# Performance work log

Measured on AMD Instinct MI355X. Metric: run time of the kernel, lower is better.

The kernel has to match this reference:

```python
import jax, jax.numpy as jnp
import numpy as np

B, N, D = 8, 2048, 256
C = 8192  # codebook_size
H = 1     # num_codebooks


def setup_inputs() -> dict:
    key = jax.random.key(0)
    k1, k2 = jax.random.split(key)
    x = jax.random.normal(k1, (B, N, D), dtype=jnp.float32)
    # kaiming_uniform_ on [H, C, D]: bound = sqrt(6 / fan_in), fan_in = C*D for a 3D tensor
    bound = float(np.sqrt(6.0 / (C * D)))
    embed = jax.random.uniform(k2, (H, C, D), dtype=jnp.float32, minval=-bound, maxval=bound)
    return {"x": x, "embed": embed}


def reference(x, embed):
    # x: [B, N, D]; module adds a codebook dim since ndim < 4, flattens to [H, B*N, D]
    flat = x.reshape(1, -1, x.shape[-1]).astype(jnp.float32)  # [H, M, D], M = B*N
    # squared euclidean distance (argmin identical to argmin of cdist p=2)
    x2 = jnp.sum(flat * flat, axis=-1, keepdims=True)              # [H, M, 1]
    e2 = jnp.sum(embed * embed, axis=-1)[:, None, :]               # [H, 1, C]
    xe = jnp.einsum('hmd,hcd->hmc', flat, embed)                   # [H, M, C]
    d2 = x2 - 2.0 * xe + e2                                        # [H, M, C]
    # sample_codebook_temp == 0 -> pure argmax of -dist == argmin of dist
    ind = jnp.argmin(d2, axis=-1)                                  # [H, M]
    quantize = jnp.take(embed[0], ind[0], axis=0).reshape(x.shape) # [B, N, D]
    embed_ind = ind.reshape(x.shape[:-1])                          # [B, N]
    return quantize, embed_ind
```

## Files before the change

### kernel.cpp

```cpp
#include <hip/hip_runtime.h>
#include <hip/hip_bf16.h>

#define M_TOT 16384
#define D_DIM 256
#define C_TOT 8192
#define NCH 4
#define CCH (C_TOT / NCH)
#define QOFF (M_TOT * D_DIM)
#define NPART 8

typedef _Float16 f16;
typedef __attribute__((ext_vector_type(8))) _Float16 f16x8;
typedef __attribute__((ext_vector_type(4))) float f32x4;

#define WS_X2 0
#define WS_E2 (M_TOT)
#define WS_BV (M_TOT + C_TOT)
#define WS_BI (WS_BV + NPART * M_TOT)
#define WS_SPL (WS_BI + NPART * M_TOT)
#define XH_OFF ((size_t)0)
#define XL_OFF ((size_t)M_TOT * D_DIM)
#define EH_OFF ((size_t)2 * M_TOT * D_DIM)
#define EL_OFF ((size_t)2 * M_TOT * D_DIM + (size_t)C_TOT * D_DIM)
#define SPL_HALFS ((size_t)2 * M_TOT * D_DIM + (size_t)2 * C_TOT * D_DIM)
#define WS_NEED ((size_t)WS_SPL * 4 + SPL_HALFS * 2)

__device__ __forceinline__ void gll16(const void* g, void* l) {
    __builtin_amdgcn_global_load_lds((const __attribute__((address_space(1))) void*)g,
                                     (__attribute__((address_space(3))) void*)l, 16, 0, 0);
}

__global__ void split_kernel(const float* __restrict__ x, const float* __restrict__ e,
                             f16* __restrict__ sp, float* __restrict__ x2, float* __restrict__ e2)
{
    int row  = blockIdx.x * 4 + (threadIdx.x >> 6);
    int lane = threadIdx.x & 63;
    bool isx = row < M_TOT;
    int r = isx ? row : row - M_TOT;
    const float* src = (isx ? x : e) + (size_t)r * D_DIM;
    float4 v = *(const float4*)(src + lane * 4);
    float s = v.x * v.x + v.y * v.y + v.z * v.z + v.w * v.w;
    #pragma unroll
    for (int off = 32; off >= 1; off >>= 1) s += __shfl_xor(s, off, 64);
    float sc = isx ? 256.0f : 16384.0f;
    float a[4] = {v.x * sc, v.y * sc, v.z * sc, v.w * sc};
    union { f16 h[4]; ushort4 u; } hh, ll;
    #pragma unroll
    for (int i = 0; i < 4; ++i) {
        f16 h = (f16)a[i];
        hh.h[i] = h;
        ll.h[i] = (f16)(a[i] - (float)h);
    }
    size_t base = (size_t)r * D_DIM + lane * 4;
    f16* ph = sp + (isx ? XH_OFF : EH_OFF) + base;
    f16* pl = sp + (isx ? XL_OFF : EL_OFF) + base;
    *(ushort4*)ph = hh.u;
    *(ushort4*)pl = ll.u;
    if (lane == 0) { if (isx) x2[r] = s; else e2[r] = s; }
}

__global__ __launch_bounds__(512, 2) void mdist_kernel(
    const f16* __restrict__ sp, const float* __restrict__ x2, const float* __restrict__ e2,
    float* __restrict__ bestv, int* __restrict__ besti)
{
    __shared__ __align__(16) f16 lds[65536];

    const int t  = threadIdx.x;
    const int l  = t & 63;
    const int wv = t >> 6;
    const int wr = wv >> 1, wc = wv & 1;
    const int mt = (int)blockIdx.x >> 2;
    const int ch = (int)blockIdx.x & 3;
    const int m0 = mt * 256, c0 = ch * CCH;

    const int q  = l >> 4;
    const int fr = l & 15;

    const int wvh = wv >> 2, rb = wv & 3;
    const f16* gxh = sp + XH_OFF + (size_t)(m0 + rb * 64 + l) * D_DIM;
    const f16* gxl = sp + XL_OFF + (size_t)(m0 + rb * 64 + l) * D_DIM;
    const f16* geh = sp + EH_OFF + (size_t)(c0 + rb * 64 + l) * D_DIM;
    const f16* gel = sp + EL_OFF + (size_t)(c0 + rb * 64 + l) * D_DIM;
    char* lbase = (char*)&lds[0] + rb * 1024 + l * 16;

#define KB(it) ((2 * (it) + wvh) & 3)
    auto STAGE = [&](int buf, int ktv, int ctv) {
        const size_t ko = (size_t)ktv * 32;
        const size_t co = (size_t)ctv * 256 * D_DIM + ko;
        char* lb = lbase + buf * 65536;
        gll16(gxh + ko + KB(0) * 8, lb + 0 * 16384 + KB(0) * 4096);
        gll16(gxh + ko + KB(1) * 8, lb + 0 * 16384 + KB(1) * 4096);
        gll16(gxl + ko + KB(2) * 8, lb + 1 * 16384 + KB(2) * 4096);
        gll16(gxl + ko + KB(3) * 8, lb + 1 * 16384 + KB(3) * 4096);
        gll16(geh + co + KB(4) * 8, lb + 2 * 16384 + KB(4) * 4096);
        gll16(geh + co + KB(5) * 8, lb + 2 * 16384 + KB(5) * 4096);
        gll16(gel + co + KB(6) * 8, lb + 3 * 16384 + KB(6) * 4096);
        gll16(gel + co + KB(7) * 8, lb + 3 * 16384 + KB(7) * 4096);
    };

    float bst[16]; int bix[16];
    #pragma unroll
    for (int i = 0; i < 16; ++i) { bst[i] = 3.4e38f; bix[i] = 0; }

    STAGE(0, 0, 0);

    for (int ct = 0; ct < 8; ++ct) {
        const int cb = c0 + ct * 256;
        f32x4 acc[4][8];
        #pragma unroll
        for (int m = 0; m < 4; ++m)
            #pragma unroll
            for (int n = 0; n < 8; ++n)
                #pragma unroll
                for (int k = 0; k < 4; ++k) acc[m][n][k] = 0.f;

        #pragma unroll 1
        for (int kt = 0; kt < 8; ++kt) {
            const int cur = kt & 1;
            asm volatile("s_waitcnt vmcnt(0)" ::: "memory");
            __syncthreads();
            __builtin_amdgcn_sched_barrier(0);

            if (kt < 7)       STAGE(cur ^ 1, kt + 1, ct);
            else if (ct < 7)  STAGE(cur ^ 1, 0, ct + 1);

            const f16* L = &lds[0] + cur * 32768;

            f16x8 ah[4], al[4];
            #pragma unroll
            for (int m = 0; m < 4; ++m) {
                int aoff = (q * 256 + wr * 64 + m * 16 + fr) * 8;
                ah[m] = *(const f16x8*)(L + aoff);
                al[m] = *(const f16x8*)(L + 8192 + aoff);
            }
            #pragma unroll
            for (int n = 0; n < 8; ++n) {
                int boff = (q * 256 + wc * 128 + n * 16 + fr) * 8;
                f16x8 bhn = *(const f16x8*)(L + 16384 + boff);
                f16x8 bln = *(const f16x8*)(L + 24576 + boff);
                __builtin_amdgcn_s_setprio(1);
                #pragma unroll
                for (int m = 0; m < 4; ++m)
                    acc[m][n] = __builtin_amdgcn_mfma_f32_16x16x32_f16(ah[m], bhn, acc[m][n], 0, 0, 0);
                #pragma unroll
                for (int m = 0; m < 4; ++m)
                    acc[m][n] = __builtin_amdgcn_mfma_f32_16x16x32_f16(ah[m], bln, acc[m][n], 0, 0, 0);
                #pragma unroll
                for (int m = 0; m < 4; ++m)
                    acc[m][n] = __builtin_amdgcn_mfma_f32_16x16x32_f16(al[m], bhn, acc[m][n], 0, 0, 0);
                __builtin_amdgcn_s_setprio(0);
            }
        }

        float e2v[8];
        #pragma unroll
        for (int n = 0; n < 8; ++n) e2v[n] = e2[cb + wc * 128 + n * 16 + fr];
        #pragma unroll
        for (int m = 0; m < 4; ++m) {
            f32x4 x2v = *(const f32x4*)(x2 + m0 + wr * 64 + m * 16 + q * 4);
            #pragma unroll
            for (int j = 0; j < 4; ++j) {
                const int bi = m * 4 + j;
                #pragma unroll
                for (int n = 0; n < 8; ++n) {
                    float d = fmaf(acc[m][n][j], -0x1p-21f, x2v[j]) + e2v[n];
                    int c = cb + wc * 128 + n * 16 + fr;
                    if (d < bst[bi]) { bst[bi] = d; bix[bi] = c; }
                }
            }
        }
    }

    #pragma unroll
    for (int i = 0; i < 16; ++i) {
        float v = bst[i]; int idx = bix[i];
        #pragma unroll
        for (int off = 8; off >= 1; off >>= 1) {
            float ov = __shfl_xor(v, off, 64);
            int   oi = __shfl_xor(idx, off, 64);
            if (ov < v || (ov == v && oi < idx)) { v = ov; idx = oi; }
        }
        if (fr == 0) {
            int row = m0 + wr * 64 + (i >> 2) * 16 + q * 4 + (i & 3);
            int p = ch * 2 + wc;
            bestv[p * M_TOT + row] = v;
            besti[p * M_TOT + row] = idx;
        }
    }
}

__global__ void finalize_kernel(const float* __restrict__ e,
                                const float* __restrict__ bestv,
                                const int* __restrict__ besti,
                                float* __restrict__ out, int npart)
{
    int m    = blockIdx.x * 4 + (threadIdx.x >> 6);
    int lane = threadIdx.x & 63;
    float bv = bestv[m]; int bi = besti[m];
    for (int h = 1; h < npart; ++h) {
        float v = bestv[h * M_TOT + m];
        int   i2 = besti[h * M_TOT + m];
        if (v < bv || (v == bv && i2 < bi)) { bv = v; bi = i2; }
    }
    if (lane == 0) out[QOFF + m] = (float)bi;
    float4 v = *(const float4*)(e + (size_t)bi * D_DIM + lane * 4);
    *(float4*)(out + (size_t)m * D_DIM + lane * 4) = v;
}

#define BMm 128
#define BNn 128
#define BKk 16
#define BSW 144
#define NKT (D_DIM / BKk)
#define NCT (CCH / BNn)

__device__ __forceinline__ int pcol(int c) { return c + ((c >> 5) << 2); }

__global__ void sq_kernel(const float* __restrict__ x, const float* __restrict__ e,
                          float* __restrict__ x2, float* __restrict__ e2) {
    int row  = blockIdx.x * 4 + (threadIdx.x >> 6);
    int lane = threadIdx.x & 63;
    const float* src = (row < M_TOT) ? (x + (size_t)row * D_DIM)
                                     : (e + (size_t)(row - M_TOT) * D_DIM);
    float4 v = *(const float4*)(src + lane * 4);
    float s = v.x * v.x + v.y * v.y + v.z * v.z + v.w * v.w;
    #pragma unroll
    for (int off = 32; off >= 1; off >>= 1) s += __shfl_xor(s, off, 64);
    if (lane == 0) { if (row < M_TOT) x2[row] = s; else e2[row - M_TOT] = s; }
}

__global__ __launch_bounds__(256, 1) void dist_kernel(
    const float* __restrict__ x, const float* __restrict__ e,
    const float* __restrict__ x2, const float* __restrict__ e2,
    float* __restrict__ bestv, int* __restrict__ besti)
{
    __shared__ __align__(16) float As[2][BKk][BMm];
    __shared__ __align__(16) float Bs[2][BKk][BSW];
    const int t  = threadIdx.x;
    const int ty = t >> 4, tx = t & 15;
    const int mt = (int)blockIdx.x >> 2;
    const int ch = (int)blockIdx.x & 3;
    const int m0 = mt * BMm, c0 = ch * CCH;
    float x2r[8];
    #pragma unroll
    for (int i = 0; i < 8; ++i) x2r[i] = x2[m0 + ty * 8 + i];
    float best[8]; int bidx[8];
    #pragma unroll
    for (int i = 0; i < 8; ++i) { best[i] = 3.4e38f; bidx[i] = 0; }
    const int r0  = t >> 2;
    const int cq0 = (t & 3) << 2;
    for (int ct = 0; ct < NCT; ++ct) {
        const int cb = c0 + ct * BNn;
        float acc[8][8];
        #pragma unroll
        for (int i = 0; i < 8; ++i)
            #pragma unroll
            for (int j = 0; j < 8; ++j) acc[i][j] = 0.f;
        #pragma unroll
        for (int it = 0; it < 2; ++it) {
            int r = r0 + it * 64;
            float4 va = *(const float4*)(x + (size_t)(m0 + r) * D_DIM + cq0);
            float4 vb = *(const float4*)(e + (size_t)(cb + r) * D_DIM + cq0);
            As[0][cq0 + 0][r] = va.x; As[0][cq0 + 1][r] = va.y;
            As[0][cq0 + 2][r] = va.z; As[0][cq0 + 3][r] = va.w;
            int pr = pcol(r);
            Bs[0][cq0 + 0][pr] = vb.x; Bs[0][cq0 + 1][pr] = vb.y;
            Bs[0][cq0 + 2][pr] = vb.z; Bs[0][cq0 + 3][pr] = vb.w;
        }
        __syncthreads();
        #pragma unroll 1
        for (int kt = 0; kt < NKT; ++kt) {
            const int cur = kt & 1;
            float4 pa[2], pb[2];
            if (kt + 1 < NKT) {
                const int k0 = (kt + 1) * BKk;
                #pragma unroll
                for (int it = 0; it < 2; ++it) {
                    int r = r0 + it * 64;
                    pa[it] = *(const float4*)(x + (size_t)(m0 + r) * D_DIM + k0 + cq0);
                    pb[it] = *(const float4*)(e + (size_t)(cb + r) * D_DIM + k0 + cq0);
                }
            }
            #pragma unroll
            for (int k = 0; k < BKk; ++k) {
                float a[8], b[8];
                *(float4*)&a[0] = *(const float4*)&As[cur][k][ty * 8];
                *(float4*)&a[4] = *(const float4*)&As[cur][k][ty * 8 + 4];
                const int pb0 = pcol(tx * 8);
                *(float4*)&b[0] = *(const float4*)&Bs[cur][k][pb0];
                *(float4*)&b[4] = *(const float4*)&Bs[cur][k][pb0 + 4];
                #pragma unroll
                for (int i = 0; i < 8; ++i)
                    #pragma unroll
                    for (int j = 0; j < 8; ++j)
                        acc[i][j] = fmaf(a[i], b[j], acc[i][j]);
            }
            __syncthreads();
            if (kt + 1 < NKT) {
                const int nb = cur ^ 1;
                #pragma unroll
                for (int it = 0; it < 2; ++it) {
                    int r = r0 + it * 64;
                    As[nb][cq0 + 0][r] = pa[it].x; As[nb][cq0 + 1][r] = pa[it].y;
                    As[nb][cq0 + 2][r] = pa[it].z; As[nb][cq0 + 3][r] = pa[it].w;
                    int pr = pcol(r);
                    Bs[nb][cq0 + 0][pr] = pb[it].x; Bs[nb][cq0 + 1][pr] = pb[it].y;
                    Bs[nb][cq0 + 2][pr] = pb[it].z; Bs[nb][cq0 + 3][pr] = pb[it].w;
                }
                __syncthreads();
            }
        }
        float e2v[8];
        #pragma unroll
        for (int j = 0; j < 8; ++j) e2v[j] = e2[cb + tx * 8 + j];
        #pragma unroll
        for (int i = 0; i < 8; ++i) {
            #pragma unroll
            for (int j = 0; j < 8; ++j) {
                float d = (x2r[i] - 2.0f * acc[i][j]) + e2v[j];
                int c = cb + tx * 8 + j;
                if (d < best[i]) { best[i] = d; bidx[i] = c; }
            }
        }
    }
    #pragma unroll
    for (int i = 0; i < 8; ++i) {
        float v = best[i]; int idx = bidx[i];
        #pragma unroll
        for (int off = 8; off >= 1; off >>= 1) {
            float ov = __shfl_xor(v, off, 64);
            int   oi = __shfl_xor(idx, off, 64);
            if (ov < v || (ov == v && oi < idx)) { v = ov; idx = oi; }
        }
        if (tx == 0) {
            int row = m0 + ty * 8 + i;
            bestv[ch * M_TOT + row] = v;
            besti[ch * M_TOT + row] = idx;
        }
    }
}

extern "C" void kernel_launch(void* const* d_in, const int* in_sizes, int n_in,
                              void* d_out, int out_size, void* d_ws, size_t ws_size,
                              hipStream_t stream) {
    const float* x = (const float*)d_in[0];
    const float* e = (const float*)d_in[1];
    float* out = (float*)d_out;

    float* wsf   = (float*)d_ws;
    float* x2    = wsf + WS_X2;
    float* e2    = wsf + WS_E2;
    float* bestv = wsf + WS_BV;
    int*   besti = (int*)(wsf + WS_BI);

    if (ws_size >= WS_NEED) {
        f16* sp = (f16*)(wsf + WS_SPL);
        split_kernel<<<(M_TOT + C_TOT) / 4, 256, 0, stream>>>(x, e, sp, x2, e2);
        mdist_kernel<<<(M_TOT / 256) * NCH, 512, 0, stream>>>(sp, x2, e2, bestv, besti);
        finalize_kernel<<<M_TOT / 4, 256, 0, stream>>>(e, bestv, besti, out, NPART);
    } else {
        sq_kernel<<<(M_TOT + C_TOT) / 4, 256, 0, stream>>>(x, e, x2, e2);
        dist_kernel<<<(M_TOT / BMm) * NCH, 256, 0, stream>>>(x, e, x2, e2, bestv, besti);
        finalize_kernel<<<M_TOT / 4, 256, 0, stream>>>(e, bestv, besti, out, NCH);
    }
}
```

Baseline: 260.0 us.

## Split K-step into four sub-phases with finer-grained staged B loads and barriers

The single per-k-step wait-all plus barrier is replaced by four sub-phases. Each sub-phase waits only on partial vmcnt and issues one slice of the next tile's B loads, so global-to-LDS prefetch is spread across the MFMA work rather than issued in one burst. The B tile LDS layout changes so that each sub-phase reads two n-columns, and the double-buffer index now runs continuously across ct iterations. This adds three extra barriers per k-step and depends on the vmcnt counts matching the number of outstanding loads exactly.

Measured after the change: 224.9 us. -13.5%, faster.

```diff
diff --git a/kernel.cpp b/kernel.cpp
--- a/kernel.cpp
+++ b/kernel.cpp
@@ -79,30 +79,39 @@
     const int wvh = wv >> 2, rb = wv & 3;
     const f16* gxh = sp + XH_OFF + (size_t)(m0 + rb * 64 + l) * D_DIM;
     const f16* gxl = sp + XL_OFF + (size_t)(m0 + rb * 64 + l) * D_DIM;
-    const f16* geh = sp + EH_OFF + (size_t)(c0 + rb * 64 + l) * D_DIM;
-    const f16* gel = sp + EL_OFF + (size_t)(c0 + rb * 64 + l) * D_DIM;
-    char* lbase = (char*)&lds[0] + rb * 1024 + l * 16;
-
-#define KB(it) ((2 * (it) + wvh) & 3)
-    auto STAGE = [&](int buf, int ktv, int ctv) {
-        const size_t ko = (size_t)ktv * 32;
-        const size_t co = (size_t)ctv * 256 * D_DIM + ko;
-        char* lb = lbase + buf * 65536;
-        gll16(gxh + ko + KB(0) * 8, lb + 0 * 16384 + KB(0) * 4096);
-        gll16(gxh + ko + KB(1) * 8, lb + 0 * 16384 + KB(1) * 4096);
-        gll16(gxl + ko + KB(2) * 8, lb + 1 * 16384 + KB(2) * 4096);
-        gll16(gxl + ko + KB(3) * 8, lb + 1 * 16384 + KB(3) * 4096);
-        gll16(geh + co + KB(4) * 8, lb + 2 * 16384 + KB(4) * 4096);
-        gll16(geh + co + KB(5) * 8, lb + 2 * 16384 + KB(5) * 4096);
-        gll16(gel + co + KB(6) * 8, lb + 3 * 16384 + KB(6) * 4096);
-        gll16(gel + co + KB(7) * 8, lb + 3 * 16384 + KB(7) * 4096);
+    const int bkb = wv & 3;
+    const f16* gB = sp + ((wv < 4) ? EH_OFF : EL_OFF)
+                    + (size_t)(c0 + (l >> 5) * 128 + (l & 31)) * D_DIM;
+    const int btn_b = (wv < 4) ? 32768 : 49152;
+
+    auto STAGE_A = [&](int buf, int ktv) {
+        char* lb = (char*)&lds[0] + buf * 65536;
+        #pragma unroll
+        for (int j = 0; j < 2; ++j) {
+            int kb = j * 2 + wvh;
+            gll16(gxh + ktv * 32 + kb * 8, lb + 0     + kb * 4096 + rb * 1024 + l * 16);
+        }
+        #pragma unroll
+        for (int j = 0; j < 2; ++j) {
+            int kb = j * 2 + wvh;
+            gll16(gxl + ktv * 32 + kb * 8, lb + 16384 + kb * 4096 + rb * 1024 + l * 16);
+        }
     };
+    auto STAGE_B = [&](int buf, int ktv, int ctv, int p) {
+        char* lb = (char*)&lds[0] + buf * 65536;
+        gll16(gB + (size_t)(ctv * 256 + 32 * p) * D_DIM + ktv * 32 + bkb * 8,
+              lb + btn_b + p * 4096 + bkb * 1024 + l * 16);
+    };
 
     float bst[16]; int bix[16];
     #pragma unroll
     for (int i = 0; i < 16; ++i) { bst[i] = 3.4e38f; bix[i] = 0; }
 
-    STAGE(0, 0, 0);
+    STAGE_A(0, 0);
+    STAGE_B(0, 0, 0, 0);
+    STAGE_B(0, 0, 0, 1);
+    STAGE_B(0, 0, 0, 2);
+    STAGE_B(0, 0, 0, 3);
 
     for (int ct = 0; ct < 8; ++ct) {
         const int cb = c0 + ct * 256;
@@ -116,38 +125,58 @@
 
         #pragma unroll 1
         for (int kt = 0; kt < 8; ++kt) {
-            const int cur = kt & 1;
-            asm volatile("s_waitcnt vmcnt(0)" ::: "memory");
-            __syncthreads();
-            __builtin_amdgcn_sched_barrier(0);
-
-            if (kt < 7)       STAGE(cur ^ 1, kt + 1, ct);
-            else if (ct < 7)  STAGE(cur ^ 1, 0, ct + 1);
-
+            const int cur = (ct * 8 + kt) & 1;
             const f16* L = &lds[0] + cur * 32768;
+            const int nbuf = cur ^ 1;
+            int nkt = kt + 1, nct = ct;
+            if (nkt == 8) { nkt = 0; nct = (ct + 1) & 7; }
 
             f16x8 ah[4], al[4];
-            #pragma unroll
-            for (int m = 0; m < 4; ++m) {
-                int aoff = (q * 256 + wr * 64 + m * 16 + fr) * 8;
-                ah[m] = *(const f16x8*)(L + aoff);
-                al[m] = *(const f16x8*)(L + 8192 + aoff);
-            }
-            #pragma unroll
-            for (int n = 0; n < 8; ++n) {
-                int boff = (q * 256 + wc * 128 + n * 16 + fr) * 8;
-                f16x8 bhn = *(const f16x8*)(L + 16384 + boff);
-                f16x8 bln = *(const f16x8*)(L + 24576 + boff);
+
+            #pragma unroll
+            for (int p = 0; p < 4; ++p) {
+                if (p == 0) asm volatile("s_waitcnt vmcnt(3)" ::: "memory");
+                else        asm volatile("s_waitcnt vmcnt(7)" ::: "memory");
+                __builtin_amdgcn_s_barrier();
+                __builtin_amdgcn_sched_barrier(0);
+
+                if (p == 0) STAGE_A(nbuf, nkt);
+                STAGE_B(nbuf, nkt, nct, p);
+
+                if (p == 0) {
+                    #pragma unroll
+                    for (int m = 0; m < 4; ++m) {
+                        int aoff = (q * 256 + wr * 64 + m * 16 + fr) * 8;
+                        ah[m] = *(const f16x8*)(L + aoff);
+                        al[m] = *(const f16x8*)(L + 8192 + aoff);
+                    }
+                }
+                const int bbase = 16384 + p * 2048 + q * 512 + wc * 256;
+                f16x8 bh0 = *(const f16x8*)(L + bbase        + (fr)      * 8);
+                f16x8 bh1 = *(const f16x8*)(L + bbase        + (16 + fr) * 8);
+                f16x8 bl0 = *(const f16x8*)(L + bbase + 8192 + (fr)      * 8);
+                f16x8 bl1 = *(const f16x8*)(L + bbase + 8192 + (16 + fr) * 8);
+                const int n0 = 2 * p, n1 = 2 * p + 1;
+
                 __builtin_amdgcn_s_setprio(1);
                 #pragma unroll
                 for (int m = 0; m < 4; ++m)
-                    acc[m][n] = __builtin_amdgcn_mfma_f32_16x16x32_f16(ah[m], bhn, acc[m][n], 0, 0, 0);
-                #pragma unroll
-                for (int m = 0; m < 4; ++m)
-                    acc[m][n] = __builtin_amdgcn_mfma_f32_16x16x32_f16(ah[m], bln, acc[m][n], 0, 0, 0);
-                #pragma unroll
-                for (int m = 0; m < 4; ++m)
-                    acc[m][n] = __builtin_amdgcn_mfma_f32_16x16x32_f16(al[m], bhn, acc[m][n], 0, 0, 0);
+                    acc[m][n0] = __builtin_amdgcn_mfma_f32_16x16x32_f16(ah[m], bh0, acc[m][n0], 0, 0, 0);
+                #pragma unroll
+                for (int m = 0; m < 4; ++m)
+                    acc[m][n1] = __builtin_amdgcn_mfma_f32_16x16x32_f16(ah[m], bh1, acc[m][n1], 0, 0, 0);
+                #pragma unroll
+                for (int m = 0; m < 4; ++m)
+                    acc[m][n0] = __builtin_amdgcn_mfma_f32_16x16x32_f16(ah[m], bl0, acc[m][n0], 0, 0, 0);
+                #pragma unroll
+                for (int m = 0; m < 4; ++m)
+                    acc[m][n1] = __builtin_amdgcn_mfma_f32_16x16x32_f16(ah[m], bl1, acc[m][n1], 0, 0, 0);
+                #pragma unroll
+                for (int m = 0; m < 4; ++m)
+                    acc[m][n0] = __builtin_amdgcn_mfma_f32_16x16x32_f16(al[m], bh0, acc[m][n0], 0, 0, 0);
+                #pragma unroll
+                for (int m = 0; m < 4; ++m)
+                    acc[m][n1] = __builtin_amdgcn_mfma_f32_16x16x32_f16(al[m], bh1, acc[m][n1], 0, 0, 0);
                 __builtin_amdgcn_s_setprio(0);
             }
         }
```

## Use 16 waves per block with 4x4 wave grid and per-row argmin reduction

Applied to the files above, without the earlier changes.

The main distance kernel grows from 8 to 16 waves per block, with each wave now covering 64x64 output tiles instead of 64x128. This halves per-wave accumulator registers and raises the number of resident waves. Staging now issues one load per operand per thread. The argmin is shuffle-reduced per row after each codebook tile, so each lane keeps one running best instead of 16. The number of partial results rises to 16 per row, which adds work to the finalize pass, and the extra cross-lane shuffles in the epilogue add overhead.

Result: slower. 351.1 us (+35.0%).

```diff
diff --git a/kernel.cpp b/kernel.cpp
--- a/kernel.cpp
+++ b/kernel.cpp
@@ -7,7 +7,7 @@
 #define NCH 4
 #define CCH (C_TOT / NCH)
 #define QOFF (M_TOT * D_DIM)
-#define NPART 8
+#define NPART 16
 
 typedef _Float16 f16;
 typedef __attribute__((ext_vector_type(8))) _Float16 f16x8;
@@ -59,7 +59,7 @@
     if (lane == 0) { if (isx) x2[r] = s; else e2[r] = s; }
 }
 
-__global__ __launch_bounds__(512, 2) void mdist_kernel(
+__global__ __launch_bounds__(1024, 4) void mdist_kernel(
     const f16* __restrict__ sp, const float* __restrict__ x2, const float* __restrict__ e2,
     float* __restrict__ bestv, int* __restrict__ besti)
 {
@@ -68,7 +68,7 @@
     const int t  = threadIdx.x;
     const int l  = t & 63;
     const int wv = t >> 6;
-    const int wr = wv >> 1, wc = wv & 1;
+    const int wr = wv >> 2, wc = wv & 3;
     const int mt = (int)blockIdx.x >> 2;
     const int ch = (int)blockIdx.x & 3;
     const int m0 = mt * 256, c0 = ch * CCH;
@@ -76,68 +76,63 @@
     const int q  = l >> 4;
     const int fr = l & 15;
 
-    const int wvh = wv >> 2, rb = wv & 3;
-    const f16* gxh = sp + XH_OFF + (size_t)(m0 + rb * 64 + l) * D_DIM;
-    const f16* gxl = sp + XL_OFF + (size_t)(m0 + rb * 64 + l) * D_DIM;
-    const f16* geh = sp + EH_OFF + (size_t)(c0 + rb * 64 + l) * D_DIM;
-    const f16* gel = sp + EL_OFF + (size_t)(c0 + rb * 64 + l) * D_DIM;
-    char* lbase = (char*)&lds[0] + rb * 1024 + l * 16;
-
-#define KB(it) ((2 * (it) + wvh) & 3)
+    const int skb = t >> 8, srow = t & 255;
+    const f16* gxh = sp + XH_OFF + (size_t)(m0 + srow) * D_DIM + skb * 8;
+    const f16* gxl = sp + XL_OFF + (size_t)(m0 + srow) * D_DIM + skb * 8;
+    const f16* geh = sp + EH_OFF + (size_t)(c0 + srow) * D_DIM + skb * 8;
+    const f16* gel = sp + EL_OFF + (size_t)(c0 + srow) * D_DIM + skb * 8;
+    const int ldst = skb * 4096 + srow * 16;
+
     auto STAGE = [&](int buf, int ktv, int ctv) {
+        char* lb = (char*)&lds[0] + buf * 65536;
         const size_t ko = (size_t)ktv * 32;
         const size_t co = (size_t)ctv * 256 * D_DIM + ko;
-        char* lb = lbase + buf * 65536;
-        gll16(gxh + ko + KB(0) * 8, lb + 0 * 16384 + KB(0) * 4096);
-        gll16(gxh + ko + KB(1) * 8, lb + 0 * 16384 + KB(1) * 4096);
-        gll16(gxl + ko + KB(2) * 8, lb + 1 * 16384 + KB(2) * 4096);
-        gll16(gxl + ko + KB(3) * 8, lb + 1 * 16384 + KB(3) * 4096);
-        gll16(geh + co + KB(4) * 8, lb + 2 * 16384 + KB(4) * 4096);
-        gll16(geh + co + KB(5) * 8, lb + 2 * 16384 + KB(5) * 4096);
-        gll16(gel + co + KB(6) * 8, lb + 3 * 16384 + KB(6) * 4096);
-        gll16(gel + co + KB(7) * 8, lb + 3 * 16384 + KB(7) * 4096);
+        gll16(gxh + ko, lb + 0     + ldst);
+        gll16(gxl + ko, lb + 16384 + ldst);
+        gll16(geh + co, lb + 32768 + ldst);
+        gll16(gel + co, lb + 49152 + ldst);
     };
 
-    float bst[16]; int bix[16];
-    #pragma unroll
-    for (int i = 0; i < 16; ++i) { bst[i] = 3.4e38f; bix[i] = 0; }
+    float bst = 3.4e38f; int bix = 0;
 
     STAGE(0, 0, 0);
 
     for (int ct = 0; ct < 8; ++ct) {
         const int cb = c0 + ct * 256;
-        f32x4 acc[4][8];
+        f32x4 acc[4][4];
         #pragma unroll
         for (int m = 0; m < 4; ++m)
             #pragma unroll
-            for (int n = 0; n < 8; ++n)
+            for (int n = 0; n < 4; ++n)
                 #pragma unroll
                 for (int k = 0; k < 4; ++k) acc[m][n][k] = 0.f;
 
         #pragma unroll 1
         for (int kt = 0; kt < 8; ++kt) {
-            const int cur = kt & 1;
+            const int cur = (ct * 8 + kt) & 1;
+            const f16* L = &lds[0] + cur * 32768;
+            const int nbuf = cur ^ 1;
+            int nkt = kt + 1, nct = ct;
+            if (nkt == 8) { nkt = 0; nct = (ct + 1) & 7; }
+
             asm volatile("s_waitcnt vmcnt(0)" ::: "memory");
-            __syncthreads();
+            __builtin_amdgcn_s_barrier();
             __builtin_amdgcn_sched_barrier(0);
 
-            if (kt < 7)       STAGE(cur ^ 1, kt + 1, ct);
-            else if (ct < 7)  STAGE(cur ^ 1, 0, ct + 1);
-
-            const f16* L = &lds[0] + cur * 32768;
+            STAGE(nbuf, nkt, nct);
 
             f16x8 ah[4], al[4];
             #pragma unroll
             for (int m = 0; m < 4; ++m) {
-                int aoff = (q * 256 + wr * 64 + m * 16 + fr) * 8;
+                int aoff = q * 2048 + (wr * 64 + m * 16 + fr) * 8;
                 ah[m] = *(const f16x8*)(L + aoff);
                 al[m] = *(const f16x8*)(L + 8192 + aoff);
             }
             #pragma unroll
-            for (int n = 0; n < 8; ++n) {
-                int boff = (q * 256 + wc * 128 + n * 16 + fr) * 8;
-                f16x8 bhn = *(const f16x8*)(L + 16384 + boff);
-                f16x8 bln = *(const f16x8*)(L + 24576 + boff);
+            for (int n = 0; n < 4; ++n) {
+                int boff = 16384 + q * 2048 + (wc * 64 + n * 16 + fr) * 8;
+                f16x8 bhn = *(const f16x8*)(L + boff);
+                f16x8 bln = *(const f16x8*)(L + 8192 + boff);
                 __builtin_amdgcn_s_setprio(1);
                 #pragma unroll
                 for (int m = 0; m < 4; ++m)
@@ -152,40 +147,40 @@
             }
         }
 
-        float e2v[8];
-        #pragma unroll
-        for (int n = 0; n < 8; ++n) e2v[n] = e2[cb + wc * 128 + n * 16 + fr];
+        float e2v[4];
+        #pragma unroll
+        for (int n = 0; n < 4; ++n) e2v[n] = e2[cb + wc * 64 + n * 16 + fr];
         #pragma unroll
         for (int m = 0; m < 4; ++m) {
-            f32x4 x2v = *(const f32x4*)(x2 + m0 + wr * 64 + m * 16 + q * 4);
             #pragma unroll
             for (int j = 0; j < 4; ++j) {
-                const int bi = m * 4 + j;
-                #pragma unroll
-                for (int n = 0; n < 8; ++n) {
-                    float d = fmaf(acc[m][n][j], -0x1p-21f, x2v[j]) + e2v[n];
-                    int c = cb + wc * 128 + n * 16 + fr;
-                    if (d < bst[bi]) { bst[bi] = d; bix[bi] = c; }
-                }
-            }
-        }
-    }
-
-    #pragma unroll
-    for (int i = 0; i < 16; ++i) {
-        float v = bst[i]; int idx = bix[i];
-        #pragma unroll
-        for (int off = 8; off >= 1; off >>= 1) {
-            float ov = __shfl_xor(v, off, 64);
-            int   oi = __shfl_xor(idx, off, 64);
-            if (ov < v || (ov == v && oi < idx)) { v = ov; idx = oi; }
-        }
-        if (fr == 0) {
-            int row = m0 + wr * 64 + (i >> 2) * 16 + q * 4 + (i & 3);
-            int p = ch * 2 + wc;
-            bestv[p * M_TOT + row] = v;
-            besti[p * M_TOT + row] = idx;
-        }
+                float xv = x2[m0 + wr * 64 + m * 16 + q * 4 + j];
+                float v = fmaf(acc[m][0][j], -0x1p-21f, xv) + e2v[0];
+                int  ci = cb + wc * 64 + fr;
+                #pragma unroll
+                for (int n = 1; n < 4; ++n) {
+                    float d = fmaf(acc[m][n][j], -0x1p-21f, xv) + e2v[n];
+                    if (d < v) { v = d; ci = cb + wc * 64 + n * 16 + fr; }
+                }
+                #pragma unroll
+                for (int off = 8; off >= 1; off >>= 1) {
+                    float ov = __shfl_xor(v, off, 64);
+                    int   oi = __shfl_xor(ci, off, 64);
+                    if (ov < v || (ov == v && oi < ci)) { v = ov; ci = oi; }
+                }
+                if ((l & 15) == m * 4 + j) {
+                    if (v < bst) { bst = v; bix = ci; }
+                }
+            }
+        }
+    }
+
+    {
+        int r   = ((l & 15) >> 2) * 16 + (l >> 4) * 4 + (l & 3);
+        int row = m0 + wr * 64 + r;
+        int p   = ch * 4 + wc;
+        bestv[p * M_TOT + row] = bst;
+        besti[p * M_TOT + row] = bix;
     }
 }
 
@@ -212,7 +207,7 @@
 #define BKk 16
 #define BSW 144
 #define NKT (D_DIM / BKk)
-#define NCT (CCH / BNn)
+#define NCTF (CCH / BNn)
 
 __device__ __forceinline__ int pcol(int c) { return c + ((c >> 5) << 2); }
 
@@ -249,7 +244,7 @@
     for (int i = 0; i < 8; ++i) { best[i] = 3.4e38f; bidx[i] = 0; }
     const int r0  = t >> 2;
     const int cq0 = (t & 3) << 2;
-    for (int ct = 0; ct < NCT; ++ct) {
+    for (int ct = 0; ct < NCTF; ++ct) {
         const int cb = c0 + ct * BNn;
         float acc[8][8];
         #pragma unroll
@@ -356,7 +351,7 @@
     if (ws_size >= WS_NEED) {
         f16* sp = (f16*)(wsf + WS_SPL);
         split_kernel<<<(M_TOT + C_TOT) / 4, 256, 0, stream>>>(x, e, sp, x2, e2);
-        mdist_kernel<<<(M_TOT / 256) * NCH, 512, 0, stream>>>(sp, x2, e2, bestv, besti);
+        mdist_kernel<<<(M_TOT / 256) * NCH, 1024, 0, stream>>>(sp, x2, e2, bestv, besti);
         finalize_kernel<<<M_TOT / 4, 256, 0, stream>>>(e, bestv, besti, out, NPART);
     } else {
         sq_kernel<<<(M_TOT + C_TOT) / 4, 256, 0, stream>>>(x, e, x2, e2);
```
